# Kernel tuning notes

Measured on AMD Instinct MI355X. Metric: run time of the kernel, lower is better.

The kernel has to match this reference:

```python
import jax, jax.numpy as jnp
import numpy as np

B, N, D = 4, 1024, 64
H, DH = 8, 64
INNER = H * DH  # 512 == dim*heads
NUM_F, GH, GW = 4, 16, 16  # N = GH*GW*NUM_F
EPS_LN = 1e-5


def setup_inputs() -> dict:
    key = jax.random.key(0)
    ks = jax.random.split(key, 5)
    return {
        "x": jax.random.normal(ks[0], (B, N, D), dtype=jnp.float32),
        "W_qkv": jax.random.normal(ks[1], (D, 3 * INNER), dtype=jnp.float32) * 0.05,
        "b_qkv": jax.random.normal(ks[2], (3 * INNER,), dtype=jnp.float32) * 0.02,
        "ln_g": jnp.ones((INNER,), dtype=jnp.float32),
        "ln_b": jnp.zeros((INNER,), dtype=jnp.float32),
        "W_out": jax.random.normal(ks[3], (INNER, D), dtype=jnp.float32) * 0.05,
        "b_out": jnp.zeros((D,), dtype=jnp.float32),
    }


def _safe_sqrt(d2):
    # sqrt with zero (not inf) gradient at 0 (diagonal of cdist)
    pos = d2 > 1e-12
    return jnp.where(pos, jnp.sqrt(jnp.where(pos, d2, 1.0)), 0.0)


def _spe_weights(x):
    # torch.cdist(x, x, p=2) then Gaussian kernel, thresholded at mean
    sq = jnp.sum(x * x, axis=-1)  # (B,N)
    d2 = sq[:, :, None] + sq[:, None, :] - 2.0 * jnp.einsum('bnd,bmd->bnm', x, x)
    d2 = jnp.maximum(d2, 0.0)
    dist = _safe_sqrt(d2)
    sigma = jnp.mean(dist)
    w = jnp.exp(-d2 / (2.0 * sigma * sigma))
    return jnp.where(w < jnp.mean(w), 0.0, w)  # (B,N,N)


def _spa_weights():
    # constant spatial-grid Gaussian weights, identical across batch
    gx, gy, gz = jnp.meshgrid(jnp.arange(GH), jnp.arange(GW), jnp.arange(NUM_F), indexing='ij')
    grid = jnp.stack([gx, gy, gz], axis=-1).reshape(N, 3).astype(jnp.float32)
    diff = grid[:, None, :] - grid[None, :, :]
    d2 = jnp.sum(diff * diff, axis=-1)
    dist = jnp.sqrt(d2)
    sigma = jnp.mean(dist)
    w = jnp.exp(-d2 / (2.0 * sigma * sigma))
    return jnp.where(w < jnp.mean(w), 0.0, w)  # (N,N)


def reference(x, W_qkv, b_qkv, ln_g, ln_b, W_out, b_out):
    spe = _spe_weights(x)            # (B,N,N), broadcast over heads
    spa = _spa_weights()             # (N,N), broadcast over batch & heads

    qkv = x @ W_qkv + b_qkv          # (B,N,3*INNER)
    q, k, v = jnp.split(qkv, 3, axis=-1)
    to_heads = lambda t: t.reshape(B, N, H, DH).transpose(0, 2, 1, 3)  # (B,H,N,DH)
    q, k, v = to_heads(q), to_heads(k), to_heads(v)

    scale = DH ** (-0.5)
    qe = jax.nn.elu(q) + 1.0
    ke = jax.nn.elu(k) + 1.0
    dots = jnp.einsum('bhid,bhjd->bhij', qe, ke) * scale  # (B,H,N,N)

    masked = dots * spe[:, None, :, :] * spa[None, None, :, :]
    attn = jax.nn.softmax(masked, axis=-1)
    out = jnp.einsum('bhij,bhjd->bhid', attn, v)          # (B,H,N,DH)
    out = out.transpose(0, 2, 1, 3).reshape(B, N, INNER)

    # to_out: LayerNorm -> GELU (exact) -> Linear
    mu = jnp.mean(out, axis=-1, keepdims=True)
    var = jnp.var(out, axis=-1, keepdims=True)
    y = ln_g * (out - mu) / jnp.sqrt(var + EPS_LN) + ln_b
    y = jax.nn.gelu(y, approximate=False)
    return y @ W_out + b_out  # (B,N,D)
```

## Files before the change

kernel.cpp:

```cpp
#include <hip/hip_runtime.h>
#include <math.h>
#include <stdlib.h>

#define B 4
#define N 1024
#define D 64
#define H 8
#define DH 64
#define INNER 512
#define C3 1536

typedef __attribute__((ext_vector_type(8))) short bf16x8;
typedef __attribute__((ext_vector_type(4))) float f32x4;

__device__ inline short f2bf(float f) {
    unsigned u = __builtin_bit_cast(unsigned, f);
    unsigned r = (u + 0x7FFFu + ((u >> 16) & 1u)) >> 16;
    return (short)r;
}
__device__ inline float bf2f(short s) {
    return __builtin_bit_cast(float, ((unsigned)(unsigned short)s) << 16);
}

__global__ __launch_bounds__(256) void k_conv(const float* __restrict__ x, const float* __restrict__ Wqkv,
                                              short* __restrict__ xh, short* __restrict__ xl,
                                              float* __restrict__ sq,
                                              short* __restrict__ Wh, short* __restrict__ Wl) {
    __shared__ float lds[64 * 65];
    int t = threadIdx.x;
    if (blockIdx.x < 1024) {
        int i = blockIdx.x * 4 + (t >> 6), d = t & 63;
        float v = x[i * 64 + d];
        short hs = f2bf(v);
        xh[i * 64 + d] = hs;
        xl[i * 64 + d] = f2bf(v - bf2f(hs));
        float s = v * v;
#pragma unroll
        for (int m = 32; m; m >>= 1) s += __shfl_xor(s, m, 64);
        if (d == 0) sq[i] = s;
    } else {
        int c0 = (blockIdx.x - 1024) * 64;
#pragma unroll
        for (int it = 0; it < 16; it++) {
            int d = it * 4 + (t >> 6), cl = t & 63;
            lds[cl * 65 + d] = Wqkv[d * C3 + c0 + cl];
        }
        __syncthreads();
#pragma unroll
        for (int it = 0; it < 16; it++) {
            int cl = it * 4 + (t >> 6), d = t & 63;
            float v = lds[cl * 65 + d];
            short hs = f2bf(v);
            Wh[(c0 + cl) * 64 + d] = hs;
            Wl[(c0 + cl) * 64 + d] = f2bf(v - bf2f(hs));
        }
    }
}

__global__ void k_spa(float* __restrict__ spa, float inv2s2, float mu) {
    int flat4 = blockIdx.x * 256 + threadIdx.x;
    int i = flat4 >> 8;
    int j0 = (flat4 & 255) * 4;
    int ix = i >> 6, iy = (i >> 2) & 15, iz = i & 3;
    float4 o;
    float* op = (float*)&o;
#pragma unroll
    for (int jj = 0; jj < 4; jj++) {
        int j = j0 + jj;
        int jx = j >> 6, jy = (j >> 2) & 15, jz = j & 3;
        float d2 = (float)((ix - jx) * (ix - jx) + (iy - jy) * (iy - jy) + (iz - jz) * (iz - jz));
        float w = expf(-d2 * inv2s2);
        op[jj] = (w < mu) ? 0.f : w;
    }
    ((float4*)spa)[flat4] = o;
}

__global__ __launch_bounds__(256) void k_qkvm(
    const short* __restrict__ xh, const short* __restrict__ xl,
    const short* __restrict__ Wh, const short* __restrict__ Wl,
    const float* __restrict__ bqkv,
    short* __restrict__ qeh, short* __restrict__ qel,
    short* __restrict__ keh, short* __restrict__ kel,
    short* __restrict__ vT) {
    __shared__ short vt_lds[128 * 66];
    int t = threadIdx.x;
    int wv = t >> 6, lane = t & 63, l4 = lane & 15, g = lane >> 4;
    int i0 = blockIdx.x * 64;
    int c0 = blockIdx.y * 128;
    int irow = i0 + wv * 16;
    const bf16x8* xh8 = (const bf16x8*)xh;
    const bf16x8* xl8 = (const bf16x8*)xl;
    const bf16x8* Wh8 = (const bf16x8*)Wh;
    const bf16x8* Wl8 = (const bf16x8*)Wl;

    int abase = (irow + l4) * 8 + g;
    bf16x8 ah[2], al[2];
    ah[0] = xh8[abase];
    ah[1] = xh8[abase + 4];
    al[0] = xl8[abase];
    al[1] = xl8[abase + 4];

    f32x4 acc[8];
#pragma unroll
    for (int ct = 0; ct < 8; ct++) acc[ct] = f32x4{0.f, 0.f, 0.f, 0.f};
#pragma unroll
    for (int ct = 0; ct < 8; ct++) {
        int c = c0 + 16 * ct + l4;
        int bbase = c * 8 + g;
        bf16x8 bh0 = Wh8[bbase], bh1 = Wh8[bbase + 4];
        bf16x8 bl0 = Wl8[bbase], bl1 = Wl8[bbase + 4];
        f32x4 a = acc[ct];
        a = __builtin_amdgcn_mfma_f32_16x16x32_bf16(ah[0], bh0, a, 0, 0, 0);
        a = __builtin_amdgcn_mfma_f32_16x16x32_bf16(ah[1], bh1, a, 0, 0, 0);
        a = __builtin_amdgcn_mfma_f32_16x16x32_bf16(al[0], bh0, a, 0, 0, 0);
        a = __builtin_amdgcn_mfma_f32_16x16x32_bf16(al[1], bh1, a, 0, 0, 0);
        a = __builtin_amdgcn_mfma_f32_16x16x32_bf16(ah[0], bl0, a, 0, 0, 0);
        a = __builtin_amdgcn_mfma_f32_16x16x32_bf16(ah[1], bl1, a, 0, 0, 0);
        acc[ct] = a;
    }
    int seg = c0 >> 9;
#pragma unroll
    for (int ct = 0; ct < 8; ct++) {
        int c = c0 + 16 * ct + l4;
        float bias = bqkv[c];
        int cc = c & 511, hh = cc >> 6, dh = cc & 63;
#pragma unroll
        for (int r = 0; r < 4; r++) {
            int i_e = irow + 4 * g + r;
            int b = i_e >> 10, i = i_e & 1023;
            float val = acc[ct][r] + bias;
            if (seg < 2) {
                float a_ = val > 0.f ? val + 1.f : __expf(val);
                short hs = f2bf(a_);
                short ls = f2bf(a_ - bf2f(hs));
                int off = ((b * H + hh) * N + i) * 64 + dh;
                if (seg == 0) { qeh[off] = hs; qel[off] = ls; }
                else          { keh[off] = hs; kel[off] = ls; }
            } else {
                vt_lds[(16 * ct + l4) * 66 + (wv * 16 + 4 * g + r)] = f2bf(val);
            }
        }
    }
    if (seg == 2) {
        __syncthreads();
        int b = i0 >> 10, ib = i0 & 1023;
#pragma unroll
        for (int it = 0; it < 4; it++) {
            int idx = t + 256 * it;
            int cl = idx >> 3, i8 = idx & 7;
            short tmp[8];
#pragma unroll
            for (int r8 = 0; r8 < 8; r8++) tmp[r8] = vt_lds[cl * 66 + i8 * 8 + r8];
            int cc = (c0 + cl) & 511, hh = cc >> 6, dh = cc & 63;
            ((bf16x8*)vT)[((b * H + hh) * 64 + dh) * (N / 8) + (ib >> 3) + i8] = *(bf16x8*)tmp;
        }
    }
}

__global__ __launch_bounds__(256) void k_gramm(
    const short* __restrict__ xh, const short* __restrict__ xl,
    const float* __restrict__ sq, float* __restrict__ w, float* __restrict__ d_sig) {
    __shared__ float red[4];
    int t = threadIdx.x;
    int wv = t >> 6, lane = t & 63, l4 = lane & 15, g = lane >> 4;
    int b = blockIdx.z;
    int i0 = blockIdx.x * 64, j0 = blockIdx.y * 128;
    int irow = i0 + wv * 16;
    const bf16x8* xh8 = (const bf16x8*)xh;
    const bf16x8* xl8 = (const bf16x8*)xl;

    int abase = (b * N + irow + l4) * 8 + g;
    bf16x8 ah[2], al[2];
    ah[0] = xh8[abase];
    ah[1] = xh8[abase + 4];
    al[0] = xl8[abase];
    al[1] = xl8[abase + 4];

    f32x4 acc[8];
#pragma unroll
    for (int ct = 0; ct < 8; ct++) acc[ct] = f32x4{0.f, 0.f, 0.f, 0.f};
#pragma unroll
    for (int ct = 0; ct < 8; ct++) {
        int j = j0 + 16 * ct + l4;
        int bbase = (b * N + j) * 8 + g;
        bf16x8 bh0 = xh8[bbase], bh1 = xh8[bbase + 4];
        bf16x8 bl0 = xl8[bbase], bl1 = xl8[bbase + 4];
        f32x4 a = acc[ct];
        a = __builtin_amdgcn_mfma_f32_16x16x32_bf16(ah[0], bh0, a, 0, 0, 0);
        a = __builtin_amdgcn_mfma_f32_16x16x32_bf16(ah[1], bh1, a, 0, 0, 0);
        a = __builtin_amdgcn_mfma_f32_16x16x32_bf16(al[0], bh0, a, 0, 0, 0);
        a = __builtin_amdgcn_mfma_f32_16x16x32_bf16(al[1], bh1, a, 0, 0, 0);
        a = __builtin_amdgcn_mfma_f32_16x16x32_bf16(ah[0], bl0, a, 0, 0, 0);
        a = __builtin_amdgcn_mfma_f32_16x16x32_bf16(ah[1], bl1, a, 0, 0, 0);
        acc[ct] = a;
    }
    float sqi[4];
#pragma unroll
    for (int r = 0; r < 4; r++) sqi[r] = sq[b * N + irow + 4 * g + r];
    float part = 0.f;
#pragma unroll
    for (int ct = 0; ct < 8; ct++) {
        int j = j0 + 16 * ct + l4;
        float sqj = sq[b * N + j];
#pragma unroll
        for (int r = 0; r < 4; r++) {
            float d2 = sqi[r] + sqj - 2.f * acc[ct][r];
            d2 = fmaxf(d2, 0.f);
            w[((size_t)b * N + irow + 4 * g + r) * N + j] = d2;
            part += (d2 > 1e-12f) ? sqrtf(d2) : 0.f;
        }
    }
#pragma unroll
    for (int m = 32; m; m >>= 1) part += __shfl_xor(part, m, 64);
    if (lane == 0) red[wv] = part;
    __syncthreads();
    if (t == 0) atomicAdd(d_sig, red[0] + red[1] + red[2] + red[3]);
}

__global__ __launch_bounds__(256) void k_wexp(float* __restrict__ w, const float* __restrict__ d_sig,
                                              float* __restrict__ d_wsum) {
    __shared__ float red[4];
    int idx = blockIdx.x * 256 + threadIdx.x;
    float sigma = d_sig[0] * (1.f / 4194304.f);
    float inv = 1.f / (2.f * sigma * sigma);
    float4 v = ((float4*)w)[idx];
    v.x = expf(-v.x * inv);
    v.y = expf(-v.y * inv);
    v.z = expf(-v.z * inv);
    v.w = expf(-v.w * inv);
    ((float4*)w)[idx] = v;
    float s = v.x + v.y + v.z + v.w;
#pragma unroll
    for (int m = 32; m; m >>= 1) s += __shfl_xor(s, m, 64);
    if ((threadIdx.x & 63) == 0) red[threadIdx.x >> 6] = s;
    __syncthreads();
    if (threadIdx.x == 0) atomicAdd(d_wsum, red[0] + red[1] + red[2] + red[3]);
}

__global__ __launch_bounds__(256) void k_attn(
    const short* __restrict__ qeh, const short* __restrict__ qel,
    const short* __restrict__ keh, const short* __restrict__ kel,
    const short* __restrict__ vT,
    const float* __restrict__ w, const float* __restrict__ spa,
    const float* __restrict__ d_wsum, float* __restrict__ aout) {
    __shared__ short Kh[64 * 64];
    __shared__ short Kl[64 * 64];
    __shared__ short Vt[64 * 64];
    __shared__ short P[4][16 * 64];
    int t = threadIdx.x;
    int wv = t >> 6, lane = t & 63, l4 = lane & 15, g = lane >> 4;
    int i0 = blockIdx.x * 64;
    int h = blockIdx.y, b = blockIdx.z, bh = b * H + h;
    float mu = d_wsum[0] * (1.f / 4194304.f);
    int irow = i0 + wv * 16;

    bf16x8 qh[2], ql[2];
    {
        const bf16x8* qh8 = (const bf16x8*)qeh;
        const bf16x8* ql8 = (const bf16x8*)qel;
        int base = (bh * N + irow + l4) * 8 + g;
#pragma unroll
        for (int mk = 0; mk < 2; mk++) {
            qh[mk] = qh8[base + 4 * mk];
            ql[mk] = ql8[base + 4 * mk];
        }
    }
    f32x4 O[4];
#pragma unroll
    for (int dt = 0; dt < 4; dt++) O[dt] = f32x4{0.f, 0.f, 0.f, 0.f};
    float m_r[4] = {-INFINITY, -INFINITY, -INFINITY, -INFINITY};
    float l_r[4] = {0.f, 0.f, 0.f, 0.f};

    const bf16x8* Kh8 = (const bf16x8*)Kh;
    const bf16x8* Kl8 = (const bf16x8*)Kl;
    const bf16x8* Vt8 = (const bf16x8*)Vt;

    for (int tile = 0; tile < 16; ++tile) {
        int j0 = tile * 64;
        __syncthreads();
        {
            const bf16x8* kh8 = (const bf16x8*)keh;
            const bf16x8* kl8 = (const bf16x8*)kel;
            const bf16x8* v8 = (const bf16x8*)vT;
            bf16x8* KhW = (bf16x8*)Kh;
            bf16x8* KlW = (bf16x8*)Kl;
            bf16x8* VtW = (bf16x8*)Vt;
#pragma unroll
            for (int rep = 0; rep < 2; rep++) {
                int c = t + 256 * rep;
                int j = c >> 3, s = c & 7;
                KhW[j * 8 + (s ^ (j & 7))] = kh8[(bh * N + j0 + j) * 8 + s];
                KlW[j * 8 + (s ^ (j & 7))] = kl8[(bh * N + j0 + j) * 8 + s];
                VtW[j * 8 + (s ^ (j & 7))] = v8[(bh * 64 + j) * (N / 8) + (j0 >> 3) + s];
            }
        }
        __syncthreads();
        f32x4 sc[4];
#pragma unroll
        for (int ct = 0; ct < 4; ct++) {
            int j = 16 * ct + l4;
            int sw = j & 7;
            bf16x8 kh0 = Kh8[j * 8 + ((g) ^ sw)];
            bf16x8 kh1 = Kh8[j * 8 + ((4 + g) ^ sw)];
            bf16x8 kl0 = Kl8[j * 8 + ((g) ^ sw)];
            bf16x8 kl1 = Kl8[j * 8 + ((4 + g) ^ sw)];
            f32x4 a = f32x4{0.f, 0.f, 0.f, 0.f};
            a = __builtin_amdgcn_mfma_f32_16x16x32_bf16(qh[0], kh0, a, 0, 0, 0);
            a = __builtin_amdgcn_mfma_f32_16x16x32_bf16(qh[1], kh1, a, 0, 0, 0);
            a = __builtin_amdgcn_mfma_f32_16x16x32_bf16(ql[0], kh0, a, 0, 0, 0);
            a = __builtin_amdgcn_mfma_f32_16x16x32_bf16(ql[1], kh1, a, 0, 0, 0);
            a = __builtin_amdgcn_mfma_f32_16x16x32_bf16(qh[0], kl0, a, 0, 0, 0);
            a = __builtin_amdgcn_mfma_f32_16x16x32_bf16(qh[1], kl1, a, 0, 0, 0);
            sc[ct] = a;
        }
        float p[4][4];
        float fr[4];
#pragma unroll
        for (int r = 0; r < 4; r++) {
            int i = irow + 4 * g + r;
            float mx = -INFINITY;
#pragma unroll
            for (int ct = 0; ct < 4; ct++) {
                int jg = j0 + 16 * ct + l4;
                float wv_ = w[((size_t)b * N + i) * N + jg];
                float sp = spa[i * N + jg];
                float spe = (wv_ < mu) ? 0.f : wv_;
                float val = sc[ct][r] * 0.125f * spe * sp;
                p[ct][r] = val;
                mx = fmaxf(mx, val);
            }
#pragma unroll
            for (int msk = 1; msk < 16; msk <<= 1) mx = fmaxf(mx, __shfl_xor(mx, msk, 64));
            float mo = m_r[r];
            float mn = fmaxf(mo, mx);
            float f = __expf(mo - mn);
            float s = 0.f;
#pragma unroll
            for (int ct = 0; ct < 4; ct++) {
                float e = __expf(p[ct][r] - mn);
                p[ct][r] = e;
                s += e;
            }
#pragma unroll
            for (int msk = 1; msk < 16; msk <<= 1) s += __shfl_xor(s, msk, 64);
            l_r[r] = l_r[r] * f + s;
            m_r[r] = mn;
            fr[r] = f;
        }
#pragma unroll
        for (int dt = 0; dt < 4; dt++) {
            O[dt][0] *= fr[0];
            O[dt][1] *= fr[1];
            O[dt][2] *= fr[2];
            O[dt][3] *= fr[3];
        }
        short* Pw = P[wv];
#pragma unroll
        for (int ct = 0; ct < 4; ct++) {
#pragma unroll
            for (int r = 0; r < 4; r++) {
                int row = 4 * g + r;
                int slot = ((l4 >> 3) + 2 * ct) ^ (row & 7);
                Pw[row * 64 + slot * 8 + (l4 & 7)] = f2bf(p[ct][r]);
            }
        }
        const bf16x8* Pr = (const bf16x8*)P[wv];
#pragma unroll
        for (int ks = 0; ks < 2; ks++) {
            bf16x8 pa = Pr[l4 * 8 + ((g + 4 * ks) ^ (l4 & 7))];
#pragma unroll
            for (int dt = 0; dt < 4; dt++) {
                int d = l4 + 16 * dt;
                bf16x8 bv = Vt8[d * 8 + ((g + 4 * ks) ^ (d & 7))];
                O[dt] = __builtin_amdgcn_mfma_f32_16x16x32_bf16(pa, bv, O[dt], 0, 0, 0);
            }
        }
    }
#pragma unroll
    for (int dt = 0; dt < 4; dt++) {
#pragma unroll
        for (int r = 0; r < 4; r++) {
            int i = irow + 4 * g + r;
            aout[((size_t)b * N + i) * INNER + h * 64 + l4 + 16 * dt] = O[dt][r] / l_r[r];
        }
    }
}

__global__ __launch_bounds__(256) void k_out(const float* __restrict__ aout, const float* __restrict__ g,
                                             const float* __restrict__ be, const float* __restrict__ Wout,
                                             const float* __restrict__ bout, float* __restrict__ out) {
    __shared__ float y_s[8 * 512];
    int t = threadIdx.x;
    int wv = t >> 6, lane = t & 63;
    int r0 = blockIdx.x * 8;
#pragma unroll
    for (int rr = 0; rr < 2; rr++) {
        int rloc = wv * 2 + rr;
        const float* rp = aout + (size_t)(r0 + rloc) * 512;
        float4 v0 = ((const float4*)rp)[lane];
        float4 v1 = ((const float4*)rp)[lane + 64];
        float s1 = v0.x + v0.y + v0.z + v0.w + v1.x + v1.y + v1.z + v1.w;
        float s2 = v0.x * v0.x + v0.y * v0.y + v0.z * v0.z + v0.w * v0.w +
                   v1.x * v1.x + v1.y * v1.y + v1.z * v1.z + v1.w * v1.w;
#pragma unroll
        for (int m = 32; m; m >>= 1) {
            s1 += __shfl_xor(s1, m, 64);
            s2 += __shfl_xor(s2, m, 64);
        }
        float mean = s1 * (1.f / 512.f);
        float var = s2 * (1.f / 512.f) - mean * mean;
        float rstd = rsqrtf(var + 1e-5f);
        int c0 = 4 * lane, c1 = 4 * lane + 256;
        float4 o0, o1;
#pragma unroll
        for (int e = 0; e < 4; e++) {
            float yn = g[c0 + e] * (((float*)&v0)[e] - mean) * rstd + be[c0 + e];
            ((float*)&o0)[e] = 0.5f * yn * (1.f + erff(yn * 0.70710678118f));
            float ym = g[c1 + e] * (((float*)&v1)[e] - mean) * rstd + be[c1 + e];
            ((float*)&o1)[e] = 0.5f * ym * (1.f + erff(ym * 0.70710678118f));
        }
        ((float4*)(y_s + rloc * 512))[lane] = o0;
        ((float4*)(y_s + rloc * 512))[lane + 64] = o1;
    }
    __syncthreads();
    int o = t & 63, rg = t >> 6;
    float a0 = 0.f, a1 = 0.f;
#pragma unroll 4
    for (int c = 0; c < 512; c++) {
        float wv_ = Wout[c * 64 + o];
        a0 = fmaf(y_s[(rg * 2) * 512 + c], wv_, a0);
        a1 = fmaf(y_s[(rg * 2 + 1) * 512 + c], wv_, a1);
    }
    float bo = bout[o];
    out[(size_t)(r0 + rg * 2) * 64 + o] = a0 + bo;
    out[(size_t)(r0 + rg * 2 + 1) * 64 + o] = a1 + bo;
}

extern "C" void kernel_launch(void* const* d_in, const int* in_sizes, int n_in,
                              void* d_out, int out_size, void* d_ws, size_t ws_size,
                              hipStream_t stream) {
    const float* x = (const float*)d_in[0];
    const float* Wqkv = (const float*)d_in[1];
    const float* bqkv = (const float*)d_in[2];
    const float* lng = (const float*)d_in[3];
    const float* lnb = (const float*)d_in[4];
    const float* Wout = (const float*)d_in[5];
    const float* bout = (const float*)d_in[6];
    float* out = (float*)d_out;

    float* ws = (float*)d_ws;
    size_t off = 0;
    float* sq = ws + off;   off += (size_t)B * N;
    float* scal = ws + off; off += 16;
    float* spa = ws + off;  off += (size_t)N * N;
    float* wbuf = ws + off; off += (size_t)B * N * N;
    float* aout = ws + off; off += (size_t)B * N * INNER;
    short* sbase = (short*)(ws + off);
    size_t soff = 0;
    short* qeh = sbase + soff; soff += (size_t)B * H * N * DH;
    short* qel = sbase + soff; soff += (size_t)B * H * N * DH;
    short* keh = sbase + soff; soff += (size_t)B * H * N * DH;
    short* kel = sbase + soff; soff += (size_t)B * H * N * DH;
    short* vT  = sbase + soff; soff += (size_t)B * H * N * DH;
    short* xh  = sbase + soff; soff += (size_t)B * N * D;
    short* xl  = sbase + soff; soff += (size_t)B * N * D;
    short* Wh  = sbase + soff; soff += (size_t)D * C3;
    short* Wl  = sbase + soff; soff += (size_t)D * C3;

    double ssum = 0.0;
    const double cnt = (double)N * (double)N;
    for (int dx = -15; dx <= 15; dx++)
        for (int dy = -15; dy <= 15; dy++)
            for (int dz = -3; dz <= 3; dz++) {
                double c = (double)(16 - abs(dx)) * (double)(16 - abs(dy)) * (double)(4 - abs(dz));
                double d2 = (double)(dx * dx + dy * dy + dz * dz);
                ssum += c * sqrt(d2);
            }
    double sigma = ssum / cnt;
    double inv2s2 = 1.0 / (2.0 * sigma * sigma);
    double wsum = 0.0;
    for (int dx = -15; dx <= 15; dx++)
        for (int dy = -15; dy <= 15; dy++)
            for (int dz = -3; dz <= 3; dz++) {
                double c = (double)(16 - abs(dx)) * (double)(16 - abs(dy)) * (double)(4 - abs(dz));
                double d2 = (double)(dx * dx + dy * dy + dz * dz);
                wsum += c * exp(-d2 * inv2s2);
            }
    double mu = wsum / cnt;

    hipMemsetAsync(scal, 0, 16 * sizeof(float), stream);
    k_conv<<<1024 + 24, 256, 0, stream>>>(x, Wqkv, xh, xl, sq, Wh, Wl);
    k_spa<<<(N * N) / 1024, 256, 0, stream>>>(spa, (float)inv2s2, (float)mu);
    k_qkvm<<<dim3(64, 12), 256, 0, stream>>>(xh, xl, Wh, Wl, bqkv, qeh, qel, keh, kel, vT);
    k_gramm<<<dim3(16, 8, B), 256, 0, stream>>>(xh, xl, sq, wbuf, scal);
    k_wexp<<<4096, 256, 0, stream>>>(wbuf, scal, scal + 1);
    k_attn<<<dim3(N / 64, H, B), 256, 0, stream>>>(qeh, qel, keh, kel, vT, wbuf, spa, scal + 1, aout);
    k_out<<<512, 256, 0, stream>>>(aout, lng, lnb, Wout, bout, out);
}
```

Measured before the change: 263.8 us.

## Split attention KV range across two blocks, merge kernels, stage mask in LDS

The attention kernel now splits the key dimension into two halves handled by separate blocks. Each block writes unnormalized partial outputs plus running max and sum, and the output kernel merges the two halves flash-decoding style before LayerNorm. The spe·spa·scale mask tile is precomputed cooperatively into shared memory instead of each lane gathering it from global memory. The prep/spa and qkv/gram kernels are fused into single launches, and expf becomes __expf. This doubles the attention grid to fill more CUs and cuts launches, at the cost of extra partial-output traffic and more LDS per block.

```diff
diff --git a/kernel.cpp b/kernel.cpp
--- a/kernel.cpp
+++ b/kernel.cpp
@@ -9,6 +9,8 @@
 #define DH 64
 #define INNER 512
 #define C3 1536
+#define BHN 32768
+#define BHND 2097152
 
 typedef __attribute__((ext_vector_type(8))) short bf16x8;
 typedef __attribute__((ext_vector_type(4))) float f32x4;
@@ -22,14 +24,16 @@
     return __builtin_bit_cast(float, ((unsigned)(unsigned short)s) << 16);
 }
 
-__global__ __launch_bounds__(256) void k_conv(const float* __restrict__ x, const float* __restrict__ Wqkv,
+__global__ __launch_bounds__(256) void k_prep(const float* __restrict__ x, const float* __restrict__ Wqkv,
                                               short* __restrict__ xh, short* __restrict__ xl,
                                               float* __restrict__ sq,
-                                              short* __restrict__ Wh, short* __restrict__ Wl) {
+                                              short* __restrict__ Wh, short* __restrict__ Wl,
+                                              float* __restrict__ spa, float inv2s2, float mu) {
     __shared__ float lds[64 * 65];
     int t = threadIdx.x;
-    if (blockIdx.x < 1024) {
-        int i = blockIdx.x * 4 + (t >> 6), d = t & 63;
+    int bb = blockIdx.x;
+    if (bb < 1024) {
+        int i = bb * 4 + (t >> 6), d = t & 63;
         float v = x[i * 64 + d];
         short hs = f2bf(v);
         xh[i * 64 + d] = hs;
@@ -38,8 +42,8 @@
 #pragma unroll
         for (int m = 32; m; m >>= 1) s += __shfl_xor(s, m, 64);
         if (d == 0) sq[i] = s;
-    } else {
-        int c0 = (blockIdx.x - 1024) * 64;
+    } else if (bb < 1048) {
+        int c0 = (bb - 1024) * 64;
 #pragma unroll
         for (int it = 0; it < 16; it++) {
             int d = it * 4 + (t >> 6), cl = t & 63;
@@ -54,167 +58,152 @@
             Wh[(c0 + cl) * 64 + d] = hs;
             Wl[(c0 + cl) * 64 + d] = f2bf(v - bf2f(hs));
         }
-    }
-}
-
-__global__ void k_spa(float* __restrict__ spa, float inv2s2, float mu) {
-    int flat4 = blockIdx.x * 256 + threadIdx.x;
-    int i = flat4 >> 8;
-    int j0 = (flat4 & 255) * 4;
-    int ix = i >> 6, iy = (i >> 2) & 15, iz = i & 3;
-    float4 o;
-    float* op = (float*)&o;
-#pragma unroll
-    for (int jj = 0; jj < 4; jj++) {
-        int j = j0 + jj;
-        int jx = j >> 6, jy = (j >> 2) & 15, jz = j & 3;
-        float d2 = (float)((ix - jx) * (ix - jx) + (iy - jy) * (iy - jy) + (iz - jz) * (iz - jz));
-        float w = expf(-d2 * inv2s2);
-        op[jj] = (w < mu) ? 0.f : w;
-    }
-    ((float4*)spa)[flat4] = o;
-}
-
-__global__ __launch_bounds__(256) void k_qkvm(
+    } else {
+        int flat4 = (bb - 1048) * 256 + t;
+        int i = flat4 >> 8;
+        int j0 = (flat4 & 255) * 4;
+        int ix = i >> 6, iy = (i >> 2) & 15, iz = i & 3;
+        float4 o;
+        float* op = (float*)&o;
+#pragma unroll
+        for (int jj = 0; jj < 4; jj++) {
+            int j = j0 + jj;
+            int jx = j >> 6, jy = (j >> 2) & 15, jz = j & 3;
+            float d2 = (float)((ix - jx) * (ix - jx) + (iy - jy) * (iy - jy) + (iz - jz) * (iz - jz));
+            float w = __expf(-d2 * inv2s2);
+            op[jj] = (w < mu) ? 0.f : w;
+        }
+        ((float4*)spa)[flat4] = o;
+    }
+}
+
+__global__ __launch_bounds__(256) void k_gemm(
     const short* __restrict__ xh, const short* __restrict__ xl,
     const short* __restrict__ Wh, const short* __restrict__ Wl,
-    const float* __restrict__ bqkv,
+    const float* __restrict__ bqkv, const float* __restrict__ sq,
     short* __restrict__ qeh, short* __restrict__ qel,
     short* __restrict__ keh, short* __restrict__ kel,
-    short* __restrict__ vT) {
+    short* __restrict__ vT, float* __restrict__ w, float* __restrict__ d_sig) {
     __shared__ short vt_lds[128 * 66];
-    int t = threadIdx.x;
-    int wv = t >> 6, lane = t & 63, l4 = lane & 15, g = lane >> 4;
-    int i0 = blockIdx.x * 64;
-    int c0 = blockIdx.y * 128;
-    int irow = i0 + wv * 16;
-    const bf16x8* xh8 = (const bf16x8*)xh;
-    const bf16x8* xl8 = (const bf16x8*)xl;
-    const bf16x8* Wh8 = (const bf16x8*)Wh;
-    const bf16x8* Wl8 = (const bf16x8*)Wl;
-
-    int abase = (irow + l4) * 8 + g;
-    bf16x8 ah[2], al[2];
-    ah[0] = xh8[abase];
-    ah[1] = xh8[abase + 4];
-    al[0] = xl8[abase];
-    al[1] = xl8[abase + 4];
-
-    f32x4 acc[8];
-#pragma unroll
-    for (int ct = 0; ct < 8; ct++) acc[ct] = f32x4{0.f, 0.f, 0.f, 0.f};
-#pragma unroll
-    for (int ct = 0; ct < 8; ct++) {
-        int c = c0 + 16 * ct + l4;
-        int bbase = c * 8 + g;
-        bf16x8 bh0 = Wh8[bbase], bh1 = Wh8[bbase + 4];
-        bf16x8 bl0 = Wl8[bbase], bl1 = Wl8[bbase + 4];
-        f32x4 a = acc[ct];
-        a = __builtin_amdgcn_mfma_f32_16x16x32_bf16(ah[0], bh0, a, 0, 0, 0);
-        a = __builtin_amdgcn_mfma_f32_16x16x32_bf16(ah[1], bh1, a, 0, 0, 0);
-        a = __builtin_amdgcn_mfma_f32_16x16x32_bf16(al[0], bh0, a, 0, 0, 0);
-        a = __builtin_amdgcn_mfma_f32_16x16x32_bf16(al[1], bh1, a, 0, 0, 0);
-        a = __builtin_amdgcn_mfma_f32_16x16x32_bf16(ah[0], bl0, a, 0, 0, 0);
-        a = __builtin_amdgcn_mfma_f32_16x16x32_bf16(ah[1], bl1, a, 0, 0, 0);
-        acc[ct] = a;
-    }
-    int seg = c0 >> 9;
-#pragma unroll
-    for (int ct = 0; ct < 8; ct++) {
-        int c = c0 + 16 * ct + l4;
-        float bias = bqkv[c];
-        int cc = c & 511, hh = cc >> 6, dh = cc & 63;
-#pragma unroll
-        for (int r = 0; r < 4; r++) {
-            int i_e = irow + 4 * g + r;
-            int b = i_e >> 10, i = i_e & 1023;
-            float val = acc[ct][r] + bias;
-            if (seg < 2) {
-                float a_ = val > 0.f ? val + 1.f : __expf(val);
-                short hs = f2bf(a_);
-                short ls = f2bf(a_ - bf2f(hs));
-                int off = ((b * H + hh) * N + i) * 64 + dh;
-                if (seg == 0) { qeh[off] = hs; qel[off] = ls; }
-                else          { keh[off] = hs; kel[off] = ls; }
-            } else {
-                vt_lds[(16 * ct + l4) * 66 + (wv * 16 + 4 * g + r)] = f2bf(val);
-            }
-        }
-    }
-    if (seg == 2) {
-        __syncthreads();
-        int b = i0 >> 10, ib = i0 & 1023;
-#pragma unroll
-        for (int it = 0; it < 4; it++) {
-            int idx = t + 256 * it;
-            int cl = idx >> 3, i8 = idx & 7;
-            short tmp[8];
-#pragma unroll
-            for (int r8 = 0; r8 < 8; r8++) tmp[r8] = vt_lds[cl * 66 + i8 * 8 + r8];
-            int cc = (c0 + cl) & 511, hh = cc >> 6, dh = cc & 63;
-            ((bf16x8*)vT)[((b * H + hh) * 64 + dh) * (N / 8) + (ib >> 3) + i8] = *(bf16x8*)tmp;
-        }
-    }
-}
-
-__global__ __launch_bounds__(256) void k_gramm(
-    const short* __restrict__ xh, const short* __restrict__ xl,
-    const float* __restrict__ sq, float* __restrict__ w, float* __restrict__ d_sig) {
     __shared__ float red[4];
     int t = threadIdx.x;
     int wv = t >> 6, lane = t & 63, l4 = lane & 15, g = lane >> 4;
-    int b = blockIdx.z;
-    int i0 = blockIdx.x * 64, j0 = blockIdx.y * 128;
-    int irow = i0 + wv * 16;
     const bf16x8* xh8 = (const bf16x8*)xh;
     const bf16x8* xl8 = (const bf16x8*)xl;
 
-    int abase = (b * N + irow + l4) * 8 + g;
-    bf16x8 ah[2], al[2];
-    ah[0] = xh8[abase];
-    ah[1] = xh8[abase + 4];
-    al[0] = xl8[abase];
-    al[1] = xl8[abase + 4];
-
-    f32x4 acc[8];
-#pragma unroll
-    for (int ct = 0; ct < 8; ct++) acc[ct] = f32x4{0.f, 0.f, 0.f, 0.f};
-#pragma unroll
-    for (int ct = 0; ct < 8; ct++) {
-        int j = j0 + 16 * ct + l4;
-        int bbase = (b * N + j) * 8 + g;
-        bf16x8 bh0 = xh8[bbase], bh1 = xh8[bbase + 4];
-        bf16x8 bl0 = xl8[bbase], bl1 = xl8[bbase + 4];
-        f32x4 a = acc[ct];
-        a = __builtin_amdgcn_mfma_f32_16x16x32_bf16(ah[0], bh0, a, 0, 0, 0);
-        a = __builtin_amdgcn_mfma_f32_16x16x32_bf16(ah[1], bh1, a, 0, 0, 0);
-        a = __builtin_amdgcn_mfma_f32_16x16x32_bf16(al[0], bh0, a, 0, 0, 0);
-        a = __builtin_amdgcn_mfma_f32_16x16x32_bf16(al[1], bh1, a, 0, 0, 0);
-        a = __builtin_amdgcn_mfma_f32_16x16x32_bf16(ah[0], bl0, a, 0, 0, 0);
-        a = __builtin_amdgcn_mfma_f32_16x16x32_bf16(ah[1], bl1, a, 0, 0, 0);
-        acc[ct] = a;
-    }
-    float sqi[4];
-#pragma unroll
-    for (int r = 0; r < 4; r++) sqi[r] = sq[b * N + irow + 4 * g + r];
-    float part = 0.f;
-#pragma unroll
-    for (int ct = 0; ct < 8; ct++) {
-        int j = j0 + 16 * ct + l4;
-        float sqj = sq[b * N + j];
-#pragma unroll
-        for (int r = 0; r < 4; r++) {
-            float d2 = sqi[r] + sqj - 2.f * acc[ct][r];
-            d2 = fmaxf(d2, 0.f);
-            w[((size_t)b * N + irow + 4 * g + r) * N + j] = d2;
-            part += (d2 > 1e-12f) ? sqrtf(d2) : 0.f;
-        }
-    }
-#pragma unroll
-    for (int m = 32; m; m >>= 1) part += __shfl_xor(part, m, 64);
-    if (lane == 0) red[wv] = part;
-    __syncthreads();
-    if (t == 0) atomicAdd(d_sig, red[0] + red[1] + red[2] + red[3]);
+    if (blockIdx.x < 768) {
+        int i0 = (blockIdx.x & 63) * 64;
+        int c0 = (blockIdx.x >> 6) * 128;
+        int irow = i0 + wv * 16;
+        const bf16x8* Wh8 = (const bf16x8*)Wh;
+        const bf16x8* Wl8 = (const bf16x8*)Wl;
+        int abase = (irow + l4) * 8 + g;
+        bf16x8 ah[2], al[2];
+        ah[0] = xh8[abase];
+        ah[1] = xh8[abase + 4];
+        al[0] = xl8[abase];
+        al[1] = xl8[abase + 4];
+        f32x4 acc[8];
+#pragma unroll
+        for (int ct = 0; ct < 8; ct++) {
+            int c = c0 + 16 * ct + l4;
+            int bbase = c * 8 + g;
+            bf16x8 bh0 = Wh8[bbase], bh1 = Wh8[bbase + 4];
+            bf16x8 bl0 = Wl8[bbase], bl1 = Wl8[bbase + 4];
+            f32x4 a = f32x4{0.f, 0.f, 0.f, 0.f};
+            a = __builtin_amdgcn_mfma_f32_16x16x32_bf16(ah[0], bh0, a, 0, 0, 0);
+            a = __builtin_amdgcn_mfma_f32_16x16x32_bf16(ah[1], bh1, a, 0, 0, 0);
+            a = __builtin_amdgcn_mfma_f32_16x16x32_bf16(al[0], bh0, a, 0, 0, 0);
+            a = __builtin_amdgcn_mfma_f32_16x16x32_bf16(al[1], bh1, a, 0, 0, 0);
+            a = __builtin_amdgcn_mfma_f32_16x16x32_bf16(ah[0], bl0, a, 0, 0, 0);
+            a = __builtin_amdgcn_mfma_f32_16x16x32_bf16(ah[1], bl1, a, 0, 0, 0);
+            acc[ct] = a;
+        }
+        int seg = c0 >> 9;
+#pragma unroll
+        for (int ct = 0; ct < 8; ct++) {
+            int c = c0 + 16 * ct + l4;
+            float bias = bqkv[c];
+            int cc = c & 511, hh = cc >> 6, dh = cc & 63;
+#pragma unroll
+            for (int r = 0; r < 4; r++) {
+                int i_e = irow + 4 * g + r;
+                int b = i_e >> 10, i = i_e & 1023;
+                float val = acc[ct][r] + bias;
+                if (seg < 2) {
+                    float a_ = val > 0.f ? val + 1.f : __expf(val);
+                    short hs = f2bf(a_);
+                    short ls = f2bf(a_ - bf2f(hs));
+                    int off = ((b * H + hh) * N + i) * 64 + dh;
+                    if (seg == 0) { qeh[off] = hs; qel[off] = ls; }
+                    else          { keh[off] = hs; kel[off] = ls; }
+                } else {
+                    vt_lds[(16 * ct + l4) * 66 + (wv * 16 + 4 * g + r)] = f2bf(val);
+                }
+            }
+        }
+        if (seg == 2) {
+            __syncthreads();
+            int b = i0 >> 10, ib = i0 & 1023;
+#pragma unroll
+            for (int it = 0; it < 4; it++) {
+                int idx = t + 256 * it;
+                int cl = idx >> 3, i8 = idx & 7;
+                short tmp[8];
+#pragma unroll
+                for (int r8 = 0; r8 < 8; r8++) tmp[r8] = vt_lds[cl * 66 + i8 * 8 + r8];
+                int cc = (c0 + cl) & 511, hh = cc >> 6, dh = cc & 63;
+                ((bf16x8*)vT)[((b * H + hh) * 64 + dh) * (N / 8) + (ib >> 3) + i8] = *(bf16x8*)tmp;
+            }
+        }
+    } else {
+        int q = blockIdx.x - 768;
+        int i0 = (q & 15) * 64, j0 = ((q >> 4) & 7) * 128, b = q >> 7;
+        int irow = i0 + wv * 16;
+        int abase = (b * N + irow + l4) * 8 + g;
+        bf16x8 ah[2], al[2];
+        ah[0] = xh8[abase];
+        ah[1] = xh8[abase + 4];
+        al[0] = xl8[abase];
+        al[1] = xl8[abase + 4];
+        f32x4 acc[8];
+#pragma unroll
+        for (int ct = 0; ct < 8; ct++) {
+            int j = j0 + 16 * ct + l4;
+            int bbase = (b * N + j) * 8 + g;
+            bf16x8 bh0 = xh8[bbase], bh1 = xh8[bbase + 4];
+            bf16x8 bl0 = xl8[bbase], bl1 = xl8[bbase + 4];
+            f32x4 a = f32x4{0.f, 0.f, 0.f, 0.f};
+            a = __builtin_amdgcn_mfma_f32_16x16x32_bf16(ah[0], bh0, a, 0, 0, 0);
+            a = __builtin_amdgcn_mfma_f32_16x16x32_bf16(ah[1], bh1, a, 0, 0, 0);
+            a = __builtin_amdgcn_mfma_f32_16x16x32_bf16(al[0], bh0, a, 0, 0, 0);
+            a = __builtin_amdgcn_mfma_f32_16x16x32_bf16(al[1], bh1, a, 0, 0, 0);
+            a = __builtin_amdgcn_mfma_f32_16x16x32_bf16(ah[0], bl0, a, 0, 0, 0);
+            a = __builtin_amdgcn_mfma_f32_16x16x32_bf16(ah[1], bl1, a, 0, 0, 0);
+            acc[ct] = a;
+        }
+        float sqi[4];
+#pragma unroll
+        for (int r = 0; r < 4; r++) sqi[r] = sq[b * N + irow + 4 * g + r];
+        float part = 0.f;
+#pragma unroll
+        for (int ct = 0; ct < 8; ct++) {
+            int j = j0 + 16 * ct + l4;
+            float sqj = sq[b * N + j];
+#pragma unroll
+            for (int r = 0; r < 4; r++) {
+                float d2 = sqi[r] + sqj - 2.f * acc[ct][r];
+                d2 = fmaxf(d2, 0.f);
+                w[((size_t)b * N + irow + 4 * g + r) * N + j] = d2;
+                part += (d2 > 1e-12f) ? sqrtf(d2) : 0.f;
+            }
+        }
+#pragma unroll
+        for (int m = 32; m; m >>= 1) part += __shfl_xor(part, m, 64);
+        if (lane == 0) red[wv] = part;
+        __syncthreads();
+        if (t == 0) atomicAdd(d_sig, red[0] + red[1] + red[2] + red[3]);
+    }
 }
 
 __global__ __launch_bounds__(256) void k_wexp(float* __restrict__ w, const float* __restrict__ d_sig,
@@ -224,10 +213,10 @@
     float sigma = d_sig[0] * (1.f / 4194304.f);
     float inv = 1.f / (2.f * sigma * sigma);
     float4 v = ((float4*)w)[idx];
-    v.x = expf(-v.x * inv);
-    v.y = expf(-v.y * inv);
-    v.z = expf(-v.z * inv);
-    v.w = expf(-v.w * inv);
+    v.x = __expf(-v.x * inv);
+    v.y = __expf(-v.y * inv);
+    v.z = __expf(-v.z * inv);
+    v.w = __expf(-v.w * inv);
     ((float4*)w)[idx] = v;
     float s = v.x + v.y + v.z + v.w;
 #pragma unroll
@@ -242,14 +231,16 @@
     const short* __restrict__ keh, const short* __restrict__ kel,
     const short* __restrict__ vT,
     const float* __restrict__ w, const float* __restrict__ spa,
-    const float* __restrict__ d_wsum, float* __restrict__ aout) {
+    const float* __restrict__ d_wsum, float* __restrict__ Opart, float2* __restrict__ ml2) {
     __shared__ short Kh[64 * 64];
     __shared__ short Kl[64 * 64];
     __shared__ short Vt[64 * 64];
     __shared__ short P[4][16 * 64];
+    __shared__ float Wm[64 * 65];
     int t = threadIdx.x;
     int wv = t >> 6, lane = t & 63, l4 = lane & 15, g = lane >> 4;
-    int i0 = blockIdx.x * 64;
+    int half = blockIdx.x & 1;
+    int i0 = (blockIdx.x >> 1) * 64;
     int h = blockIdx.y, b = blockIdx.z, bh = b * H + h;
     float mu = d_wsum[0] * (1.f / 4194304.f);
     int irow = i0 + wv * 16;
@@ -275,7 +266,7 @@
     const bf16x8* Kl8 = (const bf16x8*)Kl;
     const bf16x8* Vt8 = (const bf16x8*)Vt;
 
-    for (int tile = 0; tile < 16; ++tile) {
+    for (int tile = half * 8; tile < half * 8 + 8; ++tile) {
         int j0 = tile * 64;
         __syncthreads();
         {
@@ -292,6 +283,23 @@
                 KhW[j * 8 + (s ^ (j & 7))] = kh8[(bh * N + j0 + j) * 8 + s];
                 KlW[j * 8 + (s ^ (j & 7))] = kl8[(bh * N + j0 + j) * 8 + s];
                 VtW[j * 8 + (s ^ (j & 7))] = v8[(bh * 64 + j) * (N / 8) + (j0 >> 3) + s];
+            }
+            const float4* w4 = (const float4*)w;
+            const float4* s4 = (const float4*)spa;
+#pragma unroll
+            for (int e4 = 0; e4 < 4; e4++) {
+                int idx = t + 256 * e4;
+                int iloc = idx >> 4, j4 = idx & 15;
+                float4 wv4 = w4[((size_t)b * N + i0 + iloc) * (N / 4) + (j0 >> 2) + j4];
+                float4 sp4 = s4[(size_t)(i0 + iloc) * (N / 4) + (j0 >> 2) + j4];
+                float* wp = (float*)&wv4;
+                float* pp = (float*)&sp4;
+                float* dst = &Wm[iloc * 65 + 4 * j4];
+#pragma unroll
+                for (int e = 0; e < 4; e++) {
+                    float ww = wp[e];
+                    dst[e] = ((ww < mu) ? 0.f : ww) * pp[e] * 0.125f;
+                }
             }
         }
         __syncthreads();
@@ -317,15 +325,11 @@
         float fr[4];
 #pragma unroll
         for (int r = 0; r < 4; r++) {
-            int i = irow + 4 * g + r;
+            int rl = wv * 16 + 4 * g + r;
             float mx = -INFINITY;
 #pragma unroll
             for (int ct = 0; ct < 4; ct++) {
-                int jg = j0 + 16 * ct + l4;
-                float wv_ = w[((size_t)b * N + i) * N + jg];
-                float sp = spa[i * N + jg];
-                float spe = (wv_ < mu) ? 0.f : wv_;
-                float val = sc[ct][r] * 0.125f * spe * sp;
+                float val = sc[ct][r] * Wm[rl * 65 + 16 * ct + l4];
                 p[ct][r] = val;
                 mx = fmaxf(mx, val);
             }
@@ -376,19 +380,44 @@
             }
         }
     }
+    float* Op = Opart + (size_t)half * BHND;
 #pragma unroll
     for (int dt = 0; dt < 4; dt++) {
 #pragma unroll
         for (int r = 0; r < 4; r++) {
             int i = irow + 4 * g + r;
-            aout[((size_t)b * N + i) * INNER + h * 64 + l4 + 16 * dt] = O[dt][r] / l_r[r];
-        }
-    }
-}
-
-__global__ __launch_bounds__(256) void k_out(const float* __restrict__ aout, const float* __restrict__ g,
-                                             const float* __restrict__ be, const float* __restrict__ Wout,
-                                             const float* __restrict__ bout, float* __restrict__ out) {
+            Op[((size_t)bh * N + i) * 64 + l4 + 16 * dt] = O[dt][r];
+        }
+    }
+    if (l4 == 0) {
+#pragma unroll
+        for (int r = 0; r < 4; r++)
+            ml2[half * BHN + bh * N + irow + 4 * g + r] = float2{m_r[r], l_r[r]};
+    }
+}
+
+__device__ inline float4 comb4(const float* __restrict__ Opart, const float2* __restrict__ ml2,
+                               int bh, int ib, int dq) {
+    float2 a0 = ml2[bh * N + ib];
+    float2 a1 = ml2[BHN + bh * N + ib];
+    float m = fmaxf(a0.x, a1.x);
+    float e0 = __expf(a0.x - m), e1 = __expf(a1.x - m);
+    float inv = 1.f / (a0.y * e0 + a1.y * e1);
+    const float4* Op4 = (const float4*)Opart;
+    float4 O0 = Op4[(size_t)(bh * N + ib) * 16 + dq];
+    float4 O1 = Op4[(size_t)(BHND / 4) + (size_t)(bh * N + ib) * 16 + dq];
+    float4 v;
+    v.x = (O0.x * e0 + O1.x * e1) * inv;
+    v.y = (O0.y * e0 + O1.y * e1) * inv;
+    v.z = (O0.z * e0 + O1.z * e1) * inv;
+    v.w = (O0.w * e0 + O1.w * e1) * inv;
+    return v;
+}
+
+__global__ __launch_bounds__(256) void k_out(const float* __restrict__ Opart, const float2* __restrict__ ml2,
+                                             const float* __restrict__ g, const float* __restrict__ be,
+                                             const float* __restrict__ Wout, const float* __restrict__ bout,
+                                             float* __restrict__ out) {
     __shared__ float y_s[8 * 512];
     int t = threadIdx.x;
     int wv = t >> 6, lane = t & 63;
@@ -396,9 +425,11 @@
 #pragma unroll
     for (int rr = 0; rr < 2; rr++) {
         int rloc = wv * 2 + rr;
-        const float* rp = aout + (size_t)(r0 + rloc) * 512;
-        float4 v0 = ((const float4*)rp)[lane];
-        float4 v1 = ((const float4*)rp)[lane + 64];
+        int ig = r0 + rloc;
+        int b = ig >> 10, ib = ig & 1023;
+        int c0 = 4 * lane, c1 = c0 + 256;
+        float4 v0 = comb4(Opart, ml2, b * H + (c0 >> 6), ib, (c0 & 63) >> 2);
+        float4 v1 = comb4(Opart, ml2, b * H + (c1 >> 6), ib, (c1 & 63) >> 2);
         float s1 = v0.x + v0.y + v0.z + v0.w + v1.x + v1.y + v1.z + v1.w;
         float s2 = v0.x * v0.x + v0.y * v0.y + v0.z * v0.z + v0.w * v0.w +
                    v1.x * v1.x + v1.y * v1.y + v1.z * v1.z + v1.w * v1.w;
@@ -410,7 +441,6 @@
         float mean = s1 * (1.f / 512.f);
         float var = s2 * (1.f / 512.f) - mean * mean;
         float rstd = rsqrtf(var + 1e-5f);
-        int c0 = 4 * lane, c1 = 4 * lane + 256;
         float4 o0, o1;
 #pragma unroll
         for (int e = 0; e < 4; e++) {
@@ -450,18 +480,19 @@
 
     float* ws = (float*)d_ws;
     size_t off = 0;
-    float* sq = ws + off;   off += (size_t)B * N;
-    float* scal = ws + off; off += 16;
-    float* spa = ws + off;  off += (size_t)N * N;
-    float* wbuf = ws + off; off += (size_t)B * N * N;
-    float* aout = ws + off; off += (size_t)B * N * INNER;
+    float* sq = ws + off;    off += (size_t)B * N;
+    float* scal = ws + off;  off += 16;
+    float* spa = ws + off;   off += (size_t)N * N;
+    float* wbuf = ws + off;  off += (size_t)B * N * N;
+    float* Opart = ws + off; off += (size_t)2 * BHND;
+    float2* ml2 = (float2*)(ws + off); off += (size_t)2 * BHN * 2;
     short* sbase = (short*)(ws + off);
     size_t soff = 0;
-    short* qeh = sbase + soff; soff += (size_t)B * H * N * DH;
-    short* qel = sbase + soff; soff += (size_t)B * H * N * DH;
-    short* keh = sbase + soff; soff += (size_t)B * H * N * DH;
-    short* kel = sbase + soff; soff += (size_t)B * H * N * DH;
-    short* vT  = sbase + soff; soff += (size_t)B * H * N * DH;
+    short* qeh = sbase + soff; soff += (size_t)BHND;
+    short* qel = sbase + soff; soff += (size_t)BHND;
+    short* keh = sbase + soff; soff += (size_t)BHND;
+    short* kel = sbase + soff; soff += (size_t)BHND;
+    short* vT  = sbase + soff; soff += (size_t)BHND;
     short* xh  = sbase + soff; soff += (size_t)B * N * D;
     short* xl  = sbase + soff; soff += (size_t)B * N * D;
     short* Wh  = sbase + soff; soff += (size_t)D * C3;
@@ -489,11 +520,9 @@
     double mu = wsum / cnt;
 
     hipMemsetAsync(scal, 0, 16 * sizeof(float), stream);
-    k_conv<<<1024 + 24, 256, 0, stream>>>(x, Wqkv, xh, xl, sq, Wh, Wl);
-    k_spa<<<(N * N) / 1024, 256, 0, stream>>>(spa, (float)inv2s2, (float)mu);
-    k_qkvm<<<dim3(64, 12), 256, 0, stream>>>(xh, xl, Wh, Wl, bqkv, qeh, qel, keh, kel, vT);
-    k_gramm<<<dim3(16, 8, B), 256, 0, stream>>>(xh, xl, sq, wbuf, scal);
+    k_prep<<<2072, 256, 0, stream>>>(x, Wqkv, xh, xl, sq, Wh, Wl, spa, (float)inv2s2, (float)mu);
+    k_gemm<<<1280, 256, 0, stream>>>(xh, xl, Wh, Wl, bqkv, sq, qeh, qel, keh, kel, vT, wbuf, scal);
     k_wexp<<<4096, 256, 0, stream>>>(wbuf, scal, scal + 1);
-    k_attn<<<dim3(N / 64, H, B), 256, 0, stream>>>(qeh, qel, keh, kel, vT, wbuf, spa, scal + 1, aout);
-    k_out<<<512, 256, 0, stream>>>(aout, lng, lnb, Wout, bout, out);
-}
+    k_attn<<<dim3(32, H, B), 256, 0, stream>>>(qeh, qel, keh, kel, vT, wbuf, spa, scal + 1, Opart, ml2);
+    k_out<<<512, 256, 0, stream>>>(Opart, ml2, lng, lnb, Wout, bout, out);
+}
```

Measured after the change: 283.7 us. 1.08x slower.
